# Kernel optimization log

Measured on AMD Instinct MI355X. Metric: run time of the kernel, lower is better.

## Reference

```python
import jax, jax.numpy as jnp
import numpy as np

D_MODEL = 1024
NUM_HEADS = 16
D_K = D_MODEL // NUM_HEADS  # 64
MAX_REL_POS = 16
B, SQ, SK = 1, 2048, 2048


def setup_inputs() -> dict:
    key = jax.random.key(0)
    ks = jax.random.split(key, 12)
    s = 0.02
    inp = {
        "query": jax.random.normal(ks[0], (B, SQ, D_MODEL), jnp.float32),
        "key": jax.random.normal(ks[1], (B, SK, D_MODEL), jnp.float32),
        "value": jax.random.normal(ks[2], (B, SK, D_MODEL), jnp.float32),
        "mask": jnp.ones((B, 1, SQ, SK), dtype=bool),
        # torch nn.Linear weights: y = x @ W.T + b
        "Wq": jax.random.normal(ks[3], (D_MODEL, D_MODEL), jnp.float32) * s,
        "bq": jnp.zeros((D_MODEL,), jnp.float32),
        "Wk": jax.random.normal(ks[4], (D_MODEL, D_MODEL), jnp.float32) * s,
        "bk": jnp.zeros((D_MODEL,), jnp.float32),
        "Wv": jax.random.normal(ks[5], (D_MODEL, D_MODEL), jnp.float32) * s,
        "bv": jnp.zeros((D_MODEL,), jnp.float32),
        "Wo": jax.random.normal(ks[6], (D_MODEL, D_MODEL), jnp.float32) * s,
        "bo": jnp.zeros((D_MODEL,), jnp.float32),
        # RelativePosition embedding table: [2*P+1, d_k]
        "rel_table": jax.random.normal(ks[7], (2 * MAX_REL_POS + 1, D_K), jnp.float32) * s,
    }
    return inp


def reference(query, key, value, mask, Wq, bq, Wk, bk, Wv, bv, Wo, bo, rel_table):
    b, sq, d = query.shape
    sk = key.shape[1]
    H, dk = NUM_HEADS, D_K

    Q = (query @ Wq.T + bq).reshape(b, sq, H, dk).transpose(0, 2, 1, 3)  # [B,H,Sq,dk]
    K = (key @ Wk.T + bk).reshape(b, sk, H, dk).transpose(0, 2, 1, 3)    # [B,H,Sk,dk]
    V = (value @ Wv.T + bv).reshape(b, sk, H, dk).transpose(0, 2, 1, 3)  # [B,H,Sk,dk]

    scores = jnp.einsum("bhqd,bhkd->bhqk", Q, K)  # [B,H,Sq,Sk]

    # relative-position bias on keys: ref_pos[i,j] = clip(j-i, -P, P) + P
    pos = jnp.clip(jnp.arange(sk)[None, :] - jnp.arange(sq)[:, None],
                   -MAX_REL_POS, MAX_REL_POS) + MAX_REL_POS  # [Sq,Sk] int
    rel = rel_table[pos]  # [Sq,Sk,dk]
    scores = scores + jnp.einsum("bhqd,qkd->bhqk", Q, rel)

    scores = scores / jnp.sqrt(jnp.float32(dk))
    scores = jnp.where(mask, scores, jnp.float32(-1e12))
    attn = jax.nn.softmax(scores, axis=-1)

    x = jnp.einsum("bhqk,bhkd->bhqd", attn, V)  # [B,H,Sq,dk]
    x = x.transpose(0, 2, 1, 3).reshape(b, sq, d)
    return x @ Wo.T + bo
```

## Files before the change

kernel.cpp:

```cpp
#include <hip/hip_runtime.h>

#define S_LEN 2048
#define DM    1024
#define NH    16
#define DK    64
#define NP    33
#define QB    128
#define KB    64
#define NSPLIT 3

#define LOG2E 1.44269504088896340736f

typedef __attribute__((ext_vector_type(8))) __bf16 bf16x8;
typedef __attribute__((ext_vector_type(4))) float f32x4;
typedef __attribute__((ext_vector_type(16))) float f32x16;
typedef __attribute__((ext_vector_type(8))) unsigned short u16x8;

__device__ __forceinline__ unsigned short f2bf(float f) {
  unsigned int x = __float_as_uint(f);
  x += 0x7fffu + ((x >> 16) & 1u);
  return (unsigned short)(x >> 16);
}
__device__ __forceinline__ float bf2f(unsigned short u) {
  return __uint_as_float(((unsigned int)u) << 16);
}
__device__ __forceinline__ f32x4 mfma16(bf16x8 a, bf16x8 b, f32x4 c) {
  return __builtin_amdgcn_mfma_f32_16x16x32_bf16(a, b, c, 0, 0, 0);
}
__device__ __forceinline__ f32x16 mfma32(bf16x8 a, bf16x8 b, f32x16 c) {
  return __builtin_amdgcn_mfma_f32_32x32x16_bf16(a, b, c, 0, 0, 0);
}
__device__ __forceinline__ unsigned cvtpk(float lo, float hi) {
  unsigned r;
  asm("v_cvt_pk_bf16_f32 %0, %1, %2" : "=v"(r) : "v"(lo), "v"(hi));
  return r;
}
__device__ __forceinline__ void halfswap(unsigned &a, unsigned &b) {
  asm volatile("v_permlane32_swap_b32 %0, %1" : "+v"(a), "+v"(b));
}
__device__ __forceinline__ void gload16(const void* g, void* l) {
  __builtin_amdgcn_global_load_lds(
      (const __attribute__((address_space(1))) unsigned int*)g,
      (__attribute__((address_space(3))) unsigned int*)l, 16, 0, 0);
}
#define WAITCNT(n) asm volatile("s_waitcnt vmcnt(" #n ")" ::: "memory")
__device__ __forceinline__ void bar() { __builtin_amdgcn_s_barrier(); }

__global__ __launch_bounds__(256) void cvt_all_kernel(
    const float* q, const float* k, const float* v,
    const float* wq, const float* wk, const float* wv, const float* wo,
    unsigned short* qo, unsigned short* ko, unsigned short* vo,
    unsigned short* wqo, unsigned short* wko, unsigned short* wvo, unsigned short* woo)
{
#pragma unroll
  for (int j = 0; j < 4; j++) {
    int idx = blockIdx.x * 1024 + j * 256 + threadIdx.x;
    const float* s; unsigned short* d; int off;
    if (idx < 786432) {
      int sel = idx >> 18; off = idx & 262143;
      s = sel == 0 ? q : (sel == 1 ? k : v);
      d = sel == 0 ? qo : (sel == 1 ? ko : vo);
    } else {
      int w = idx - 786432;
      int sel = w >> 17; off = w & 131071;
      s = sel == 0 ? wq : (sel == 1 ? wk : (sel == 2 ? wv : wo));
      d = sel == 0 ? wqo : (sel == 1 ? wko : (sel == 2 ? wvo : woo));
    }
    const float* p = s + (size_t)off * 8;
    u16x8 o;
#pragma unroll
    for (int e = 0; e < 8; e++) o[e] = f2bf(p[e]);
    *(u16x8*)(d + (size_t)off * 8) = o;
  }
}

template<int MR, int NR, int F32OUT>
__device__ __forceinline__ void gemm_body(
    const unsigned short* __restrict__ A, const unsigned short* __restrict__ W,
    const float* __restrict__ bias, unsigned short* __restrict__ outb,
    float* __restrict__ outf, int N, int K, int bm, int bn, float scale)
{
  __shared__ unsigned short As[2][MR * 32 * 64];
  __shared__ unsigned short Bs[2][NR * 32 * 64];
  int tid = threadIdx.x, lane = tid & 63, w = tid >> 6;
  int r15 = lane & 15, g = lane >> 4;
  int wm = (w & 1) * (MR * 16), wn = (w >> 1) * (NR * 16);
  f32x4 acc[MR][NR];
#pragma unroll
  for (int mi = 0; mi < MR; mi++)
#pragma unroll
    for (int ni = 0; ni < NR; ni++)
#pragma unroll
      for (int i = 0; i < 4; i++) acc[mi][ni][i] = 0.f;

  int lc = w * 64 + lane;
  int lrow = lc >> 3;
  int lk = ((lc & 7) ^ (lrow & 7)) * 8;
  const unsigned short* aS = &A[(size_t)(bm + lrow) * K + lk];
  const unsigned short* bS = &W[(size_t)(bn + lrow) * K + lk];
  int wOff = w * 512;

  auto STAGE = [&](int b, int k0) {
#pragma unroll
    for (int j = 0; j < MR; j++)
      gload16(aS + (size_t)(32 * j) * K + k0, &As[b][j * 2048 + wOff]);
#pragma unroll
    for (int j = 0; j < NR; j++)
      gload16(bS + (size_t)(32 * j) * K + k0, &Bs[b][j * 2048 + wOff]);
  };

  const int NS = K / 64;
  STAGE(0, 0);
  WAITCNT(0);
  bar();
  for (int s = 0; s < NS; s++) {
    int cur = s & 1;
    int k0 = s * 64;
    if (s + 1 < NS) STAGE(cur ^ 1, k0 + 64);
    bf16x8 af[MR][2], bfr[NR][2];
#pragma unroll
    for (int mi = 0; mi < MR; mi++) {
      int row = wm + mi * 16 + r15;
#pragma unroll
      for (int hf = 0; hf < 2; hf++)
        af[mi][hf] = *(const bf16x8*)&As[cur][row * 64 + (((hf * 4 + g) ^ (row & 7)) << 3)];
    }
#pragma unroll
    for (int ni = 0; ni < NR; ni++) {
      int row = wn + ni * 16 + r15;
#pragma unroll
      for (int hf = 0; hf < 2; hf++)
        bfr[ni][hf] = *(const bf16x8*)&Bs[cur][row * 64 + (((hf * 4 + g) ^ (row & 7)) << 3)];
    }
    __builtin_amdgcn_s_setprio(1);
#pragma unroll
    for (int hf = 0; hf < 2; hf++)
#pragma unroll
      for (int mi = 0; mi < MR; mi++)
#pragma unroll
        for (int ni = 0; ni < NR; ni++)
          acc[mi][ni] = mfma16(af[mi][hf], bfr[ni][hf], acc[mi][ni]);
    __builtin_amdgcn_s_setprio(0);
    WAITCNT(0);
    bar();
  }
#pragma unroll
  for (int mi = 0; mi < MR; mi++)
#pragma unroll
    for (int ni = 0; ni < NR; ni++) {
      int col = bn + wn + ni * 16 + r15;
      float bv = bias[col];
#pragma unroll
      for (int i = 0; i < 4; i++) {
        int row = bm + wm + mi * 16 + g * 4 + i;
        float v = (acc[mi][ni][i] + bv) * scale;
        if (F32OUT) outf[(size_t)row * N + col] = v;
        else        outb[(size_t)row * N + col] = f2bf(v);
      }
    }
}

__global__ __launch_bounds__(256, 3) void gemm_qkv_kernel(
    const unsigned short* X0, const unsigned short* X1, const unsigned short* X2,
    const unsigned short* W0, const unsigned short* W1, const unsigned short* W2,
    const float* b0, const float* b1, const float* b2,
    unsigned short* O0, unsigned short* O1, unsigned short* O2)
{
  int z = blockIdx.z;
  const unsigned short* A = z == 0 ? X0 : (z == 1 ? X1 : X2);
  const unsigned short* W = z == 0 ? W0 : (z == 1 ? W1 : W2);
  const float* bias       = z == 0 ? b0 : (z == 1 ? b1 : b2);
  unsigned short* O       = z == 0 ? O0 : (z == 1 ? O1 : O2);
  float scale             = z == 0 ? 0.125f * LOG2E : 1.f;
  gemm_body<2, 4, 0>(A, W, bias, O, nullptr, DM, DM, blockIdx.y * 64, blockIdx.x * 128, scale);
}

__global__ __launch_bounds__(256, 2) void gemm_out_kernel(
    const unsigned short* A, const unsigned short* W, const float* bias, float* out)
{
  gemm_body<2, 2, 1>(A, W, bias, nullptr, out, DM, DM, blockIdx.y * 64, blockIdx.x * 64, 1.f);
}

__global__ __launch_bounds__(256) void prep_kernel(
    const unsigned short* __restrict__ Vb, unsigned short* __restrict__ VT,
    const unsigned short* __restrict__ Qb, const float* __restrict__ rel,
    unsigned short* __restrict__ QRbT)
{
  int h = blockIdx.y;
  int tid = threadIdx.x;
  if (blockIdx.x < 32) {
    __shared__ unsigned short Tl[64 * 64];
    int k0 = blockIdx.x * 64;
#pragma unroll
    for (int i = 0; i < 2; i++) {
      int c = tid + i * 256;
      int r = c >> 3, ch = c & 7;
      u16x8 v = *(const u16x8*)&Vb[(size_t)(k0 + r) * DM + h * DK + ch * 8];
      *(u16x8*)&Tl[r * 64 + ((ch ^ (r & 7)) << 3)] = v;
    }
    __syncthreads();
#pragma unroll
    for (int i = 0; i < 2; i++) {
      int c = tid + i * 256;
      int d = c >> 3, k8 = (c & 7) * 8;
      u16x8 o;
#pragma unroll
      for (int j = 0; j < 8; j++) {
        int row = k8 + j;
        o[j] = Tl[row * 64 + (((d >> 3) ^ (row & 7)) << 3) + (d & 7)];
      }
      *(u16x8*)&VT[((size_t)h * DK + d) * S_LEN + k0 + k8] = o;
    }
  } else {
    __shared__ float rels[NP * DK];
    int q = (blockIdx.x - 32) * 256 + tid;
    for (int i = tid; i < NP * DK; i += 256) rels[i] = rel[i];
    __syncthreads();
    float qv[DK];
    const unsigned short* qp = &Qb[(size_t)q * DM + h * DK];
#pragma unroll
    for (int j = 0; j < 8; j++) {
      u16x8 v = *(const u16x8*)&qp[j * 8];
#pragma unroll
      for (int e = 0; e < 8; e++) qv[j * 8 + e] = bf2f(v[e]);
    }
    int qt = q >> 7, qloc = q & 127;
    unsigned short* outp = &QRbT[((size_t)(h * 16 + qt) * NP) * QB + qloc];
    for (int p = 0; p < NP; p++) {
      float s = 0.f;
#pragma unroll
      for (int d = 0; d < DK; d++) s += qv[d] * rels[p * DK + d];
      outp[p * QB] = f2bf(s);
    }
  }
}

__global__ __launch_bounds__(256, 3) void attn_kernel(
    const unsigned short* __restrict__ Qb, const unsigned short* __restrict__ Kb,
    const unsigned short* __restrict__ VT, const unsigned short* __restrict__ QRbT,
    unsigned short* __restrict__ Opart, float* __restrict__ ml)
{
  __shared__ unsigned short Ks[2][KB * DK];
  __shared__ unsigned short Vs[2][DK * KB];
  __shared__ unsigned short QRs[NP * QB];

  int bid = blockIdx.x;
  int wid = (bid & 7) * 96 + (bid >> 3);
  int h  = wid / 48;
  int rem = wid - h * 48;
  int split = rem >> 4;
  int qt = rem & 15;
  int q0 = qt * QB;
  int tstart = split * 11;
  int ts = split == 2 ? 10 : 11;

  int tid = threadIdx.x;
  int l = tid & 63, w = tid >> 6;
  int lq = l & 31, hi = l >> 5;

  int c0 = tid, c1 = tid + 256;
  int r0 = c0 >> 3, s0 = ((c0 & 7) ^ (r0 & 7)) * 8;
  int r1 = c1 >> 3, s1 = ((c1 & 7) ^ (r1 & 7)) * 8;
  int db0 = w * 512, db1 = 2048 + w * 512;
  const unsigned short* Ksrc0 = &Kb[(size_t)r0 * DM + h * DK + s0];
  const unsigned short* Ksrc1 = &Kb[(size_t)r1 * DM + h * DK + s1];
  const unsigned short* Vsrc0 = &VT[((size_t)h * DK + r0) * S_LEN + s0];
  const unsigned short* Vsrc1 = &VT[((size_t)h * DK + r1) * S_LEN + s1];

  auto STAGE = [&](int buf, int kb) {
    gload16(Ksrc0 + (size_t)kb * DM, &Ks[buf][db0]);
    gload16(Ksrc1 + (size_t)kb * DM, &Ks[buf][db1]);
    gload16(Vsrc0 + kb, &Vs[buf][db0]);
    gload16(Vsrc1 + kb, &Vs[buf][db1]);
  };

  int kb0 = tstart * KB;
  STAGE(0, kb0);

  {
    const u16x8* qsrc = (const u16x8*)&QRbT[(size_t)(h * 16 + qt) * NP * QB];
    u16x8* qdst = (u16x8*)QRs;
    for (int i = tid; i < NP * QB / 8; i += 256) qdst[i] = qsrc[i];
  }

  int qglob = q0 + w * 32 + lq;
  int qcol = w * 32 + lq;
  const unsigned short* qp = &Qb[(size_t)qglob * DM + h * DK + hi * 8];
  bf16x8 qfs[4];
#pragma unroll
  for (int s = 0; s < 4; s++) qfs[s] = *(const bf16x8*)&qp[s * 16];

  float m_i = -1e30f, l_i = 0.f;
  f32x16 o0, o1;
#pragma unroll
  for (int r = 0; r < 16; r++) { o0[r] = 0.f; o1[r] = 0.f; }

  asm volatile("s_waitcnt vmcnt(0) lgkmcnt(0)" ::: "memory");
  bar();

  for (int t = 0; t < ts; t++) {
    int buf = t & 1;
    int kbase = (tstart + t) * KB;
    if (t + 1 < ts) STAGE(buf ^ 1, kbase + KB);

    f32x16 sT0, sT1;
#pragma unroll
    for (int r = 0; r < 16; r++) { sT0[r] = 0.f; sT1[r] = 0.f; }
    __builtin_amdgcn_s_setprio(1);
#pragma unroll
    for (int s = 0; s < 4; s++) {
      int ch = s * 2 + hi;
      bf16x8 k0 = *(const bf16x8*)&Ks[buf][(lq) * DK + ((ch ^ (lq & 7)) << 3)];
      bf16x8 k1 = *(const bf16x8*)&Ks[buf][(32 + lq) * DK + ((ch ^ (lq & 7)) << 3)];
      sT0 = mfma32(k0, qfs[s], sT0);
      sT1 = mfma32(k1, qfs[s], sT1);
    }
    __builtin_amdgcn_s_setprio(0);

    bool hiC = (kbase - (q0 + QB - 1)) >= 16;
    bool loC = ((kbase + KB - 1) - q0) <= -16;
    float c_u = 0.f;
    if (hiC || loC) {
      c_u = bf2f(QRs[(hiC ? 32 : 0) * QB + qcol]);
    } else {
#pragma unroll
      for (int r = 0; r < 16; r++) {
        int km = (r & 3) + ((r >> 2) << 3) + (hi << 2);
        int d0 = kbase + km - qglob;
        int i0 = d0 < -16 ? 0 : (d0 > 16 ? 32 : d0 + 16);
        sT0[r] += bf2f(QRs[i0 * QB + qcol]);
        int d1 = d0 + 32;
        int i1 = d1 < -16 ? 0 : (d1 > 16 ? 32 : d1 + 16);
        sT1[r] += bf2f(QRs[i1 * QB + qcol]);
      }
    }

    float a0 = fmaxf(sT0[0], sT1[0]), a1 = fmaxf(sT0[1], sT1[1]);
    float a2 = fmaxf(sT0[2], sT1[2]), a3 = fmaxf(sT0[3], sT1[3]);
#pragma unroll
    for (int r = 4; r < 16; r += 4) {
      a0 = fmaxf(a0, fmaxf(sT0[r], sT1[r]));
      a1 = fmaxf(a1, fmaxf(sT0[r + 1], sT1[r + 1]));
      a2 = fmaxf(a2, fmaxf(sT0[r + 2], sT1[r + 2]));
      a3 = fmaxf(a3, fmaxf(sT0[r + 3], sT1[r + 3]));
    }
    float tm = fmaxf(fmaxf(a0, a1), fmaxf(a2, a3));
    tm = fmaxf(tm, __shfl_xor(tm, 32));
    float eff = tm + c_u;
    if (!__all(eff <= m_i + 11.5f)) {
      float mn = fmaxf(m_i, eff);
      float sc = __builtin_amdgcn_exp2f(m_i - mn);
      m_i = mn; l_i *= sc;
#pragma unroll
      for (int r = 0; r < 16; r++) { o0[r] *= sc; o1[r] *= sc; }
    }
    float mc = m_i - c_u;
    float p[32];
    float ls0 = 0.f, ls1 = 0.f, ls2 = 0.f, ls3 = 0.f;
#pragma unroll
    for (int r = 0; r < 16; r += 4) {
      p[r]     = __builtin_amdgcn_exp2f(sT0[r] - mc);     ls0 += p[r];
      p[r + 1] = __builtin_amdgcn_exp2f(sT0[r + 1] - mc); ls1 += p[r + 1];
      p[r + 2] = __builtin_amdgcn_exp2f(sT0[r + 2] - mc); ls2 += p[r + 2];
      p[r + 3] = __builtin_amdgcn_exp2f(sT0[r + 3] - mc); ls3 += p[r + 3];
    }
#pragma unroll
    for (int r = 0; r < 16; r += 4) {
      p[16 + r]     = __builtin_amdgcn_exp2f(sT1[r] - mc);     ls0 += p[16 + r];
      p[16 + r + 1] = __builtin_amdgcn_exp2f(sT1[r + 1] - mc); ls1 += p[16 + r + 1];
      p[16 + r + 2] = __builtin_amdgcn_exp2f(sT1[r + 2] - mc); ls2 += p[16 + r + 2];
      p[16 + r + 3] = __builtin_amdgcn_exp2f(sT1[r + 3] - mc); ls3 += p[16 + r + 3];
    }
    float ls = (ls0 + ls1) + (ls2 + ls3);
    ls += __shfl_xor(ls, 32);
    l_i += ls;

    bf16x8 pf[4];
#pragma unroll
    for (int kg = 0; kg < 2; kg++) {
      const float* pp = &p[kg * 16];
#pragma unroll
      for (int s2 = 0; s2 < 2; s2++) {
        unsigned b1 = cvtpk(pp[s2 * 8 + 0], pp[s2 * 8 + 1]);
        unsigned b2 = cvtpk(pp[s2 * 8 + 4], pp[s2 * 8 + 5]);
        unsigned b3 = cvtpk(pp[s2 * 8 + 2], pp[s2 * 8 + 3]);
        unsigned b4 = cvtpk(pp[s2 * 8 + 6], pp[s2 * 8 + 7]);
        halfswap(b1, b2); halfswap(b3, b4);
        union { unsigned u[4]; bf16x8 v; } f;
        f.u[0] = b1; f.u[1] = b3; f.u[2] = b2; f.u[3] = b4;
        pf[kg * 2 + s2] = f.v;
      }
    }

    __builtin_amdgcn_s_setprio(1);
#pragma unroll
    for (int s = 0; s < 4; s++) {
      int ch = s * 2 + hi;
      bf16x8 v0 = *(const bf16x8*)&Vs[buf][(lq) * KB + ((ch ^ (lq & 7)) << 3)];
      bf16x8 v1 = *(const bf16x8*)&Vs[buf][(32 + lq) * KB + ((ch ^ (lq & 7)) << 3)];
      o0 = mfma32(v0, pf[s], o0);
      o1 = mfma32(v1, pf[s], o1);
    }
    __builtin_amdgcn_s_setprio(0);

    WAITCNT(0);
    bar();
  }

  float inv = 1.f / l_i;
  unsigned* Ot32 = (unsigned*)Ks;
  int qloc = w * 32 + lq;
  int swz = (qloc & 7) << 3;
#pragma unroll
  for (int r = 0; r < 16; r += 2) {
    int d0 = (r & 3) + ((r >> 2) << 3) + (hi << 2);
    Ot32[qloc * 32 + (((d0) ^ swz) >> 1)]      = cvtpk(o0[r] * inv, o0[r + 1] * inv);
    Ot32[qloc * 32 + (((d0 + 32) ^ swz) >> 1)] = cvtpk(o1[r] * inv, o1[r + 1] * inv);
  }
  __syncthreads();
  unsigned short* Ot = (unsigned short*)Ks;
  size_t pb = ((size_t)(h * 16 + qt) * NSPLIT + split) * QB;
#pragma unroll
  for (int i = 0; i < 4; i++) {
    int c = i * 256 + tid;
    int q = c >> 3, ch = c & 7;
    *(u16x8*)&Opart[(pb + q) * DK + ch * 8] =
        *(const u16x8*)&Ot[q * 64 + ((ch ^ (q & 7)) << 3)];
  }
  if (hi == 0) {
    float2 v; v.x = m_i; v.y = l_i;
    *(float2*)&ml[(pb + qloc) * 2] = v;
  }
}

__global__ __launch_bounds__(256) void merge_kernel(
    const unsigned short* __restrict__ Opart, const float* __restrict__ ml,
    unsigned short* __restrict__ Xb)
{
  __shared__ float wsc[NSPLIT][QB];
  int qt = blockIdx.x, h = blockIdx.y;
  int tid = threadIdx.x;
  size_t pb = (size_t)(h * 16 + qt) * NSPLIT;
  if (tid < QB) {
    float m[NSPLIT], li[NSPLIT];
#pragma unroll
    for (int s = 0; s < NSPLIT; s++) {
      float2 v = *(const float2*)&ml[((pb + s) * QB + tid) * 2];
      m[s] = v.x; li[s] = v.y;
    }
    float mx = fmaxf(fmaxf(m[0], m[1]), m[2]);
    float t[NSPLIT], sum = 0.f;
#pragma unroll
    for (int s = 0; s < NSPLIT; s++) { t[s] = exp2f(m[s] - mx) * li[s]; sum += t[s]; }
    float inv = 1.f / sum;
#pragma unroll
    for (int s = 0; s < NSPLIT; s++) wsc[s][tid] = t[s] * inv;
  }
  __syncthreads();
  int q0 = qt * QB;
#pragma unroll
  for (int i = 0; i < 4; i++) {
    int c = i * 256 + tid;
    int q = c >> 3, d8 = (c & 7) * 8;
    float acc[8];
#pragma unroll
    for (int j = 0; j < 8; j++) acc[j] = 0.f;
#pragma unroll
    for (int s = 0; s < NSPLIT; s++) {
      u16x8 v = *(const u16x8*)&Opart[((pb + s) * QB + q) * DK + d8];
      float ws = wsc[s][q];
#pragma unroll
      for (int j = 0; j < 8; j++) acc[j] += ws * bf2f(v[j]);
    }
    u16x8 o;
#pragma unroll
    for (int j = 0; j < 8; j++) o[j] = f2bf(acc[j]);
    *(u16x8*)&Xb[(size_t)(q0 + q) * DM + h * DK + d8] = o;
  }
}

extern "C" void kernel_launch(void* const* d_in, const int* in_sizes, int n_in,
                              void* d_out, int out_size, void* d_ws, size_t ws_size,
                              hipStream_t stream) {
  const float* query = (const float*)d_in[0];
  const float* key_  = (const float*)d_in[1];
  const float* value = (const float*)d_in[2];
  const float* Wq = (const float*)d_in[4];
  const float* bq = (const float*)d_in[5];
  const float* Wk = (const float*)d_in[6];
  const float* bk = (const float*)d_in[7];
  const float* Wv = (const float*)d_in[8];
  const float* bv = (const float*)d_in[9];
  const float* Wo = (const float*)d_in[10];
  const float* bo = (const float*)d_in[11];
  const float* rel = (const float*)d_in[12];

  char* ws = (char*)d_ws;
  unsigned short* qin = (unsigned short*)(ws + 0);
  unsigned short* kin = (unsigned short*)(ws + 4194304);
  unsigned short* vin = (unsigned short*)(ws + 8388608);
  unsigned short* Wqb = (unsigned short*)(ws + 12582912);
  unsigned short* Wkb = (unsigned short*)(ws + 14680064);
  unsigned short* Wvb = (unsigned short*)(ws + 16777216);
  unsigned short* Wob = (unsigned short*)(ws + 18874368);
  unsigned short* Qb  = (unsigned short*)(ws + 20971520);
  unsigned short* Kb  = (unsigned short*)(ws + 25165824);
  unsigned short* Vb  = (unsigned short*)(ws + 29360128);
  unsigned short* Xb  = (unsigned short*)(ws + 33554432);
  unsigned short* QRb = (unsigned short*)(ws + 37748736);
  unsigned short* VT  = (unsigned short*)(ws + 41943040);
  unsigned short* Opart = (unsigned short*)(ws + 0);
  float* mlbuf = (float*)(ws + 12582912);

  cvt_all_kernel<<<dim3(1280), dim3(256), 0, stream>>>(
      query, key_, value, Wq, Wk, Wv, Wo, qin, kin, vin, Wqb, Wkb, Wvb, Wob);

  gemm_qkv_kernel<<<dim3(8, 32, 3), dim3(256), 0, stream>>>(
      qin, kin, vin, Wqb, Wkb, Wvb, bq, bk, bv, Qb, Kb, Vb);

  prep_kernel<<<dim3(40, 16), dim3(256), 0, stream>>>(Vb, VT, Qb, rel, QRb);

  attn_kernel<<<dim3(768), dim3(256), 0, stream>>>(Qb, Kb, VT, QRb, Opart, mlbuf);
  merge_kernel<<<dim3(16, 16), dim3(256), 0, stream>>>(Opart, mlbuf, Xb);

  gemm_out_kernel<<<dim3(16, 32), dim3(256), 0, stream>>>(Xb, Wob, bo, (float*)d_out);
}
```

Baseline: 100.1 us.

## Fuse fp32-to-bf16 input conversion and V transpose into QKV projection GEMM

The QKV GEMM now reads fp32 activations directly, converting them to bf16 in registers before writing to LDS, so the separate conversion pass over query/key/value is dropped. The V projection epilogue transposes its tile through shared memory and writes V^T directly, which removes the transpose half of the prep kernel. Weight conversion stays as its own small kernel. The trade-off is that the GEMM's A operand now doubles its global read bytes and is loaded through registers rather than async LDS loads, which may expose latency.

```diff
diff --git a/kernel.cpp b/kernel.cpp
--- a/kernel.cpp
+++ b/kernel.cpp
@@ -44,33 +44,166 @@
       (__attribute__((address_space(3))) unsigned int*)l, 16, 0, 0);
 }
 #define WAITCNT(n) asm volatile("s_waitcnt vmcnt(" #n ")" ::: "memory")
+#define LGKM0 asm volatile("s_waitcnt lgkmcnt(0)" ::: "memory")
 __device__ __forceinline__ void bar() { __builtin_amdgcn_s_barrier(); }
-
-__global__ __launch_bounds__(256) void cvt_all_kernel(
-    const float* q, const float* k, const float* v,
+__device__ __forceinline__ u16x8 pk8(float4 a, float4 b) {
+  union { unsigned u[4]; u16x8 v; } f;
+  f.u[0] = cvtpk(a.x, a.y); f.u[1] = cvtpk(a.z, a.w);
+  f.u[2] = cvtpk(b.x, b.y); f.u[3] = cvtpk(b.z, b.w);
+  return f.v;
+}
+
+__global__ __launch_bounds__(256) void cvt_w_kernel(
     const float* wq, const float* wk, const float* wv, const float* wo,
-    unsigned short* qo, unsigned short* ko, unsigned short* vo,
     unsigned short* wqo, unsigned short* wko, unsigned short* wvo, unsigned short* woo)
 {
 #pragma unroll
   for (int j = 0; j < 4; j++) {
     int idx = blockIdx.x * 1024 + j * 256 + threadIdx.x;
-    const float* s; unsigned short* d; int off;
-    if (idx < 786432) {
-      int sel = idx >> 18; off = idx & 262143;
-      s = sel == 0 ? q : (sel == 1 ? k : v);
-      d = sel == 0 ? qo : (sel == 1 ? ko : vo);
-    } else {
-      int w = idx - 786432;
-      int sel = w >> 17; off = w & 131071;
-      s = sel == 0 ? wq : (sel == 1 ? wk : (sel == 2 ? wv : wo));
-      d = sel == 0 ? wqo : (sel == 1 ? wko : (sel == 2 ? wvo : woo));
-    }
+    int sel = idx >> 17, off = idx & 131071;
+    const float* s = sel == 0 ? wq : (sel == 1 ? wk : (sel == 2 ? wv : wo));
+    unsigned short* d = sel == 0 ? wqo : (sel == 1 ? wko : (sel == 2 ? wvo : woo));
     const float* p = s + (size_t)off * 8;
     u16x8 o;
 #pragma unroll
     for (int e = 0; e < 8; e++) o[e] = f2bf(p[e]);
     *(u16x8*)(d + (size_t)off * 8) = o;
+  }
+}
+
+__global__ __launch_bounds__(256, 3) void gemm_qkv_kernel(
+    const float* X0, const float* X1, const float* X2,
+    const unsigned short* W0, const unsigned short* W1, const unsigned short* W2,
+    const float* b0, const float* b1, const float* b2,
+    unsigned short* O0, unsigned short* O1, unsigned short* VTout)
+{
+  __shared__ unsigned short As[2][64 * 64];
+  __shared__ unsigned short Bs[2][128 * 64];
+  int z = blockIdx.z;
+  const float* A          = z == 0 ? X0 : (z == 1 ? X1 : X2);
+  const unsigned short* W = z == 0 ? W0 : (z == 1 ? W1 : W2);
+  const float* bias       = z == 0 ? b0 : (z == 1 ? b1 : b2);
+  float scale             = z == 0 ? 0.125f * LOG2E : 1.f;
+  int bm = blockIdx.y * 64, bn = blockIdx.x * 128;
+
+  int tid = threadIdx.x, lane = tid & 63, w = tid >> 6;
+  int r15 = lane & 15, g = lane >> 4;
+  int wm = (w & 1) * 32, wn = (w >> 1) * 64;
+  f32x4 acc[2][4];
+#pragma unroll
+  for (int mi = 0; mi < 2; mi++)
+#pragma unroll
+    for (int ni = 0; ni < 4; ni++)
+#pragma unroll
+      for (int i = 0; i < 4; i++) acc[mi][ni][i] = 0.f;
+
+  int ra0 = tid >> 3, sa0 = ((tid & 7) ^ (ra0 & 7)) * 8;
+  int ra1 = ra0 + 32, sa1 = (((tid + 256) & 7) ^ (ra1 & 7)) * 8;
+  const float* aF0 = &A[(size_t)(bm + ra0) * DM + sa0];
+  const float* aF1 = &A[(size_t)(bm + ra1) * DM + sa1];
+  const unsigned short* bSrc[4];
+#pragma unroll
+  for (int j = 0; j < 4; j++) {
+    int cb = j * 256 + tid;
+    int rb = cb >> 3, sb = ((cb & 7) ^ (rb & 7)) * 8;
+    bSrc[j] = &W[(size_t)(bn + rb) * DM + sb];
+  }
+
+  float4 a00, a01, a10, a11;
+  auto LOAD_A = [&](int k0) {
+    a00 = *(const float4*)(aF0 + k0);     a01 = *(const float4*)(aF0 + k0 + 4);
+    a10 = *(const float4*)(aF1 + k0);     a11 = *(const float4*)(aF1 + k0 + 4);
+  };
+  auto STAGE_B = [&](int b, int k0) {
+#pragma unroll
+    for (int j = 0; j < 4; j++) gload16(bSrc[j] + k0, &Bs[b][(j * 256 + tid) * 8]);
+  };
+  auto WRITE_A = [&](int b) {
+    *(u16x8*)&As[b][tid * 8]         = pk8(a00, a01);
+    *(u16x8*)&As[b][(tid + 256) * 8] = pk8(a10, a11);
+  };
+
+  const int NS = DM / 64;
+  STAGE_B(0, 0);
+  LOAD_A(0);
+  WAITCNT(0);
+  WRITE_A(0);
+  LGKM0;
+  bar();
+
+  for (int s = 0; s < NS; s++) {
+    int cur = s & 1;
+    int k0 = s * 64;
+    if (s + 1 < NS) { STAGE_B(cur ^ 1, k0 + 64); LOAD_A(k0 + 64); }
+    bf16x8 af[2][2], bfr[4][2];
+#pragma unroll
+    for (int mi = 0; mi < 2; mi++) {
+      int row = wm + mi * 16 + r15;
+#pragma unroll
+      for (int hf = 0; hf < 2; hf++)
+        af[mi][hf] = *(const bf16x8*)&As[cur][row * 64 + (((hf * 4 + g) ^ (row & 7)) << 3)];
+    }
+#pragma unroll
+    for (int ni = 0; ni < 4; ni++) {
+      int row = wn + ni * 16 + r15;
+#pragma unroll
+      for (int hf = 0; hf < 2; hf++)
+        bfr[ni][hf] = *(const bf16x8*)&Bs[cur][row * 64 + (((hf * 4 + g) ^ (row & 7)) << 3)];
+    }
+    __builtin_amdgcn_s_setprio(1);
+#pragma unroll
+    for (int hf = 0; hf < 2; hf++)
+#pragma unroll
+      for (int mi = 0; mi < 2; mi++)
+#pragma unroll
+        for (int ni = 0; ni < 4; ni++)
+          acc[mi][ni] = mfma16(af[mi][hf], bfr[ni][hf], acc[mi][ni]);
+    __builtin_amdgcn_s_setprio(0);
+    if (s + 1 < NS) {
+      WAITCNT(0);
+      WRITE_A(cur ^ 1);
+    }
+    LGKM0;
+    bar();
+  }
+
+  if (z < 2) {
+    unsigned short* O = z == 0 ? O0 : O1;
+#pragma unroll
+    for (int mi = 0; mi < 2; mi++)
+#pragma unroll
+      for (int ni = 0; ni < 4; ni++) {
+        int col = bn + wn + ni * 16 + r15;
+        float bv = bias[col];
+#pragma unroll
+        for (int i = 0; i < 4; i++) {
+          int row = bm + wm + mi * 16 + g * 4 + i;
+          O[(size_t)row * DM + col] = f2bf((acc[mi][ni][i] + bv) * scale);
+        }
+      }
+  } else {
+    unsigned short* Tl = (unsigned short*)Bs;
+    const int TP = 72;
+#pragma unroll
+    for (int mi = 0; mi < 2; mi++)
+#pragma unroll
+      for (int ni = 0; ni < 4; ni++) {
+        int colL = wn + ni * 16 + r15;
+        float bv = bias[bn + colL];
+#pragma unroll
+        for (int i = 0; i < 4; i++) {
+          int rowL = wm + mi * 16 + g * 4 + i;
+          Tl[colL * TP + rowL] = f2bf(acc[mi][ni][i] + bv);
+        }
+      }
+    __syncthreads();
+#pragma unroll
+    for (int i = 0; i < 4; i++) {
+      int c = i * 256 + tid;
+      int colL = c >> 3, k8 = (c & 7) * 8;
+      u16x8 vv = *(const u16x8*)&Tl[colL * TP + k8];
+      *(u16x8*)&VTout[(size_t)(bn + colL) * S_LEN + bm + k8] = vv;
+    }
   }
 }
 
@@ -160,78 +293,37 @@
     }
 }
 
-__global__ __launch_bounds__(256, 3) void gemm_qkv_kernel(
-    const unsigned short* X0, const unsigned short* X1, const unsigned short* X2,
-    const unsigned short* W0, const unsigned short* W1, const unsigned short* W2,
-    const float* b0, const float* b1, const float* b2,
-    unsigned short* O0, unsigned short* O1, unsigned short* O2)
-{
-  int z = blockIdx.z;
-  const unsigned short* A = z == 0 ? X0 : (z == 1 ? X1 : X2);
-  const unsigned short* W = z == 0 ? W0 : (z == 1 ? W1 : W2);
-  const float* bias       = z == 0 ? b0 : (z == 1 ? b1 : b2);
-  unsigned short* O       = z == 0 ? O0 : (z == 1 ? O1 : O2);
-  float scale             = z == 0 ? 0.125f * LOG2E : 1.f;
-  gemm_body<2, 4, 0>(A, W, bias, O, nullptr, DM, DM, blockIdx.y * 64, blockIdx.x * 128, scale);
-}
-
 __global__ __launch_bounds__(256, 2) void gemm_out_kernel(
     const unsigned short* A, const unsigned short* W, const float* bias, float* out)
 {
   gemm_body<2, 2, 1>(A, W, bias, nullptr, out, DM, DM, blockIdx.y * 64, blockIdx.x * 64, 1.f);
 }
 
-__global__ __launch_bounds__(256) void prep_kernel(
-    const unsigned short* __restrict__ Vb, unsigned short* __restrict__ VT,
+__global__ __launch_bounds__(256) void qrel_kernel(
     const unsigned short* __restrict__ Qb, const float* __restrict__ rel,
     unsigned short* __restrict__ QRbT)
 {
+  __shared__ float rels[NP * DK];
   int h = blockIdx.y;
   int tid = threadIdx.x;
-  if (blockIdx.x < 32) {
-    __shared__ unsigned short Tl[64 * 64];
-    int k0 = blockIdx.x * 64;
-#pragma unroll
-    for (int i = 0; i < 2; i++) {
-      int c = tid + i * 256;
-      int r = c >> 3, ch = c & 7;
-      u16x8 v = *(const u16x8*)&Vb[(size_t)(k0 + r) * DM + h * DK + ch * 8];
-      *(u16x8*)&Tl[r * 64 + ((ch ^ (r & 7)) << 3)] = v;
-    }
-    __syncthreads();
-#pragma unroll
-    for (int i = 0; i < 2; i++) {
-      int c = tid + i * 256;
-      int d = c >> 3, k8 = (c & 7) * 8;
-      u16x8 o;
-#pragma unroll
-      for (int j = 0; j < 8; j++) {
-        int row = k8 + j;
-        o[j] = Tl[row * 64 + (((d >> 3) ^ (row & 7)) << 3) + (d & 7)];
-      }
-      *(u16x8*)&VT[((size_t)h * DK + d) * S_LEN + k0 + k8] = o;
-    }
-  } else {
-    __shared__ float rels[NP * DK];
-    int q = (blockIdx.x - 32) * 256 + tid;
-    for (int i = tid; i < NP * DK; i += 256) rels[i] = rel[i];
-    __syncthreads();
-    float qv[DK];
-    const unsigned short* qp = &Qb[(size_t)q * DM + h * DK];
-#pragma unroll
-    for (int j = 0; j < 8; j++) {
-      u16x8 v = *(const u16x8*)&qp[j * 8];
-#pragma unroll
-      for (int e = 0; e < 8; e++) qv[j * 8 + e] = bf2f(v[e]);
-    }
-    int qt = q >> 7, qloc = q & 127;
-    unsigned short* outp = &QRbT[((size_t)(h * 16 + qt) * NP) * QB + qloc];
-    for (int p = 0; p < NP; p++) {
-      float s = 0.f;
-#pragma unroll
-      for (int d = 0; d < DK; d++) s += qv[d] * rels[p * DK + d];
-      outp[p * QB] = f2bf(s);
-    }
+  int q = blockIdx.x * 256 + tid;
+  for (int i = tid; i < NP * DK; i += 256) rels[i] = rel[i];
+  __syncthreads();
+  float qv[DK];
+  const unsigned short* qp = &Qb[(size_t)q * DM + h * DK];
+#pragma unroll
+  for (int j = 0; j < 8; j++) {
+    u16x8 v = *(const u16x8*)&qp[j * 8];
+#pragma unroll
+    for (int e = 0; e < 8; e++) qv[j * 8 + e] = bf2f(v[e]);
+  }
+  int qt = q >> 7, qloc = q & 127;
+  unsigned short* outp = &QRbT[((size_t)(h * 16 + qt) * NP) * QB + qloc];
+  for (int p = 0; p < NP; p++) {
+    float s = 0.f;
+#pragma unroll
+    for (int d = 0; d < DK; d++) s += qv[d] * rels[p * DK + d];
+    outp[p * QB] = f2bf(s);
   }
 }
 
@@ -496,29 +588,25 @@
   const float* rel = (const float*)d_in[12];
 
   char* ws = (char*)d_ws;
-  unsigned short* qin = (unsigned short*)(ws + 0);
-  unsigned short* kin = (unsigned short*)(ws + 4194304);
-  unsigned short* vin = (unsigned short*)(ws + 8388608);
-  unsigned short* Wqb = (unsigned short*)(ws + 12582912);
-  unsigned short* Wkb = (unsigned short*)(ws + 14680064);
-  unsigned short* Wvb = (unsigned short*)(ws + 16777216);
-  unsigned short* Wob = (unsigned short*)(ws + 18874368);
-  unsigned short* Qb  = (unsigned short*)(ws + 20971520);
-  unsigned short* Kb  = (unsigned short*)(ws + 25165824);
-  unsigned short* Vb  = (unsigned short*)(ws + 29360128);
-  unsigned short* Xb  = (unsigned short*)(ws + 33554432);
-  unsigned short* QRb = (unsigned short*)(ws + 37748736);
-  unsigned short* VT  = (unsigned short*)(ws + 41943040);
   unsigned short* Opart = (unsigned short*)(ws + 0);
   float* mlbuf = (float*)(ws + 12582912);
-
-  cvt_all_kernel<<<dim3(1280), dim3(256), 0, stream>>>(
-      query, key_, value, Wq, Wk, Wv, Wo, qin, kin, vin, Wqb, Wkb, Wvb, Wob);
+  unsigned short* Wqb = (unsigned short*)(ws + 13369344);
+  unsigned short* Wkb = (unsigned short*)(ws + 15466496);
+  unsigned short* Wvb = (unsigned short*)(ws + 17563648);
+  unsigned short* Wob = (unsigned short*)(ws + 19660800);
+  unsigned short* Qb  = (unsigned short*)(ws + 21757952);
+  unsigned short* Kb  = (unsigned short*)(ws + 25952256);
+  unsigned short* VT  = (unsigned short*)(ws + 30146560);
+  unsigned short* Xb  = (unsigned short*)(ws + 34340864);
+  unsigned short* QRb = (unsigned short*)(ws + 38535168);
+
+  cvt_w_kernel<<<dim3(512), dim3(256), 0, stream>>>(
+      Wq, Wk, Wv, Wo, Wqb, Wkb, Wvb, Wob);
 
   gemm_qkv_kernel<<<dim3(8, 32, 3), dim3(256), 0, stream>>>(
-      qin, kin, vin, Wqb, Wkb, Wvb, bq, bk, bv, Qb, Kb, Vb);
-
-  prep_kernel<<<dim3(40, 16), dim3(256), 0, stream>>>(Vb, VT, Qb, rel, QRb);
+      query, key_, value, Wqb, Wkb, Wvb, bq, bk, bv, Qb, Kb, VT);
+
+  qrel_kernel<<<dim3(8, 16), dim3(256), 0, stream>>>(Qb, rel, QRb);
 
   attn_kernel<<<dim3(768), dim3(256), 0, stream>>>(Qb, Kb, VT, QRb, Opart, mlbuf);
   merge_kernel<<<dim3(16, 16), dim3(256), 0, stream>>>(Opart, mlbuf, Xb);
```

New measurement: 104.8 us. 4.7% more time.
